# Kernel tuning notes

Hardware: AMD Instinct MI355X
Metric: run time of the kernel (lower is better)

The kernel has to match this reference:

```python
import math
import jax, jax.numpy as jnp
import numpy as np

B, N, D, H = 4, 2048, 512, 8
HD = D // H


def setup_inputs() -> dict:
    key = jax.random.key(0)
    ks = jax.random.split(key, 7)
    w_scale = 1.0 / math.sqrt(D)  # keep logits in a sane range (like default init)
    return {
        "q": jax.random.normal(ks[0], (B, N, D), dtype=jnp.float32),
        "mask": jax.random.randint(ks[1], (B, N), 0, 2) == 1,  # True = masked key
        "attn_bias": jax.random.normal(ks[2], (B, N, N), dtype=jnp.float32),
        "Wq": jax.random.normal(ks[3], (D, D), dtype=jnp.float32) * w_scale,
        "Wk": jax.random.normal(ks[4], (D, D), dtype=jnp.float32) * w_scale,
        "Wv": jax.random.normal(ks[5], (D, D), dtype=jnp.float32) * w_scale,
        "Wo": jax.random.normal(ks[6], (D, D), dtype=jnp.float32) * w_scale,
    }


def _heads(v):
    # [B, N, D] -> [H, B, N, HD]  (mirrors reshape + movedim(-2, 0))
    b, n, d = v.shape
    return v.reshape(b, n, H, HD).transpose(2, 0, 1, 3)


def reference(q, mask, attn_bias, Wq, Wk, Wv, Wo):
    # Linear projections (torch Linear: x @ W.T)
    qh = _heads(q @ Wq.T)
    kh = _heads(q @ Wk.T)   # self-attention: h defaults to q
    vh = _heads(q @ Wv.T)
    # scores: [H, B, Nq, Nk]
    scores = jnp.einsum("hbqd,hbkd->hbqk", qh, kh) / math.sqrt(HD)
    scores = scores + attn_bias[None]                     # broadcast over heads
    scores = jnp.where(mask[None, :, None, :], -jnp.inf, scores)
    attn = jax.nn.softmax(scores, axis=-1)
    out = jnp.einsum("hbqk,hbkd->hbqd", attn, vh)         # [H, B, Nq, HD]
    out = out.transpose(1, 2, 0, 3).reshape(q.shape[0], q.shape[1], D)
    return out @ Wo.T
```

## Files before the change

### kernel.cpp

```cpp
#include <hip/hip_runtime.h>
#include <stdint.h>


typedef __attribute__((ext_vector_type(8))) short short8;
typedef __attribute__((ext_vector_type(4))) short short4v;
typedef __attribute__((ext_vector_type(4))) float f32x4;

#define DEV static __device__ __forceinline__

constexpr int Bc = 4, Nc = 2048, Dc = 512, Hc = 8, HDc = 64;
constexpr int Mc = Bc * Nc;
constexpr int QKVNc = 3 * Dc;
constexpr float L2E = 1.44269504f;

DEV short bf16cast(float f) {
  return (short)__builtin_bit_cast(unsigned short, (__bf16)f);
}
DEV unsigned cvt_pk_bf16(float a, float b) {
  unsigned short lb = __builtin_bit_cast(unsigned short, (__bf16)a);
  unsigned short hb = __builtin_bit_cast(unsigned short, (__bf16)b);
  return (unsigned)lb | ((unsigned)hb << 16);
}
DEV unsigned pack_shorts(short a, short b) {
  return (unsigned)(unsigned short)a | ((unsigned)(unsigned short)b << 16);
}
DEV short8 cvt8(float4 a, float4 b) {
  union { short8 s; uint4 u; } r;
  r.u.x = cvt_pk_bf16(a.x, a.y); r.u.y = cvt_pk_bf16(a.z, a.w);
  r.u.z = cvt_pk_bf16(b.x, b.y); r.u.w = cvt_pk_bf16(b.z, b.w);
  return r.s;
}
DEV float fast_exp2(float x) {
#if __has_builtin(__builtin_amdgcn_exp2f)
  return __builtin_amdgcn_exp2f(x);
#else
  return exp2f(x);
#endif
}
DEV void permswap32(unsigned& a, unsigned& b) {
  asm volatile("v_permlane32_swap_b32 %0, %1" : "+v"(a), "+v"(b));
}

__global__ void cvtw_kernel(const float* __restrict__ Wq, const float* __restrict__ Wk,
                            const float* __restrict__ Wv, const float* __restrict__ Wo,
                            short* __restrict__ Wqkv, short* __restrict__ Wob) {
  int which = blockIdx.x >> 8;
  int j = (blockIdx.x & 255) * 256 + threadIdx.x;
  const float* src = which == 0 ? Wq : which == 1 ? Wk : which == 2 ? Wv : Wo;
  short* dst = (which == 3) ? Wob : Wqkv + which * (Dc * Dc);
  float4 v = ((const float4*)src)[j];
  short4v o = { bf16cast(v.x), bf16cast(v.y), bf16cast(v.z), bf16cast(v.w) };
  ((short4v*)dst)[j] = o;
}

__global__ void maskprep_kernel(const void* __restrict__ mask, float* __restrict__ mf) {
  __shared__ int flag;
  if (threadIdx.x == 0) flag = 0;
  __syncthreads();
  const uchar4* m4 = (const uchar4*)mask;
  int acc = 0;
  for (int i = threadIdx.x; i < 2048; i += 1024) {
    uchar4 v = m4[i];
    acc |= (int)v.y | (int)v.z | (int)v.w;
  }
  if (acc) atomicOr(&flag, 1);
  __syncthreads();
  int isbyte = flag;
  for (int i = threadIdx.x; i < Bc * Nc; i += 1024) {
    int v = isbyte ? (int)((const unsigned char*)mask)[i] : ((const int*)mask)[i];
    mf[i] = v ? -1e30f : 0.0f;
  }
}

template<bool A_F32, bool OUT_F32>
__global__ __launch_bounds__(256, 2) void gemm_bt(const void* __restrict__ Av,
                                                  const short* __restrict__ Bm,
                                                  void* __restrict__ Cv,
                                                  int M, int N, int K,
                                                  int qcols, float cscale) {
  __shared__ __align__(16) short At[128 * 72];
  __shared__ __align__(16) short Bt[128 * 72];
  const int tid = threadIdx.x, lane = tid & 63, wv = tid >> 6;
  const int quad = lane >> 4, l16 = lane & 15;
  const int mbase = blockIdx.y * 128, nbase = blockIdx.x * 128;
  const int wr = (wv >> 1) * 64, wc = (wv & 1) * 64;
  const float scale = (nbase < qcols) ? cscale : 1.0f;
  f32x4 acc[4][4] = {};
  float4 apf[4][2]; short8 aph[4], bpre[4];
#pragma unroll
  for (int i = 0; i < 4; i++) {
    int flat = i * 256 + tid, row = flat >> 3, ch8 = (flat & 7) * 8;
    if (A_F32) {
      const float* Af = (const float*)Av;
      apf[i][0] = *(const float4*)&Af[(size_t)(mbase + row) * K + ch8];
      apf[i][1] = *(const float4*)&Af[(size_t)(mbase + row) * K + ch8 + 4];
    } else {
      aph[i] = *(const short8*)&((const short*)Av)[(size_t)(mbase + row) * K + ch8];
    }
    bpre[i] = *(const short8*)&Bm[(size_t)(nbase + row) * K + ch8];
  }
  for (int k0 = 0; k0 < K; k0 += 64) {
    __syncthreads();
#pragma unroll
    for (int i = 0; i < 4; i++) {
      int flat = i * 256 + tid, row = flat >> 3, ch8 = (flat & 7) * 8;
      *(short8*)&At[row * 72 + ch8] = A_F32 ? cvt8(apf[i][0], apf[i][1]) : aph[i];
      *(short8*)&Bt[row * 72 + ch8] = bpre[i];
    }
    if (k0 + 64 < K) {
#pragma unroll
      for (int i = 0; i < 4; i++) {
        int flat = i * 256 + tid, row = flat >> 3, ch8 = (flat & 7) * 8;
        if (A_F32) {
          const float* Af = (const float*)Av;
          apf[i][0] = *(const float4*)&Af[(size_t)(mbase + row) * K + k0 + 64 + ch8];
          apf[i][1] = *(const float4*)&Af[(size_t)(mbase + row) * K + k0 + 64 + ch8 + 4];
        } else {
          aph[i] = *(const short8*)&((const short*)Av)[(size_t)(mbase + row) * K + k0 + 64 + ch8];
        }
        bpre[i] = *(const short8*)&Bm[(size_t)(nbase + row) * K + k0 + 64 + ch8];
      }
    }
    __syncthreads();
#pragma unroll
    for (int s = 0; s < 2; s++) {
      short8 af[4], bf[4];
#pragma unroll
      for (int t = 0; t < 4; t++) {
        af[t] = *(short8*)&At[(wr + t * 16 + l16) * 72 + quad * 8 + s * 32];
        bf[t] = *(short8*)&Bt[(wc + t * 16 + l16) * 72 + quad * 8 + s * 32];
      }
#pragma unroll
      for (int mt = 0; mt < 4; mt++)
#pragma unroll
        for (int nt = 0; nt < 4; nt++)
          acc[mt][nt] = __builtin_amdgcn_mfma_f32_16x16x32_bf16(af[mt], bf[nt], acc[mt][nt], 0, 0, 0);
    }
  }
#pragma unroll
  for (int mt = 0; mt < 4; mt++)
#pragma unroll
    for (int nt = 0; nt < 4; nt++)
#pragma unroll
      for (int r = 0; r < 4; r++) {
        int row = mbase + wr + mt * 16 + quad * 4 + r;
        int col = nbase + wc + nt * 16 + l16;
        float v = acc[mt][nt][r] * scale;
        if (OUT_F32) ((float*)Cv)[(size_t)row * N + col] = v;
        else         ((short*)Cv)[(size_t)row * N + col] = bf16cast(v);
      }
}

__global__ __launch_bounds__(256, 2) void attn_kernel(const short* __restrict__ QKV,
                                                      const float* __restrict__ bias,
                                                      const float* __restrict__ maskf,
                                                      short* __restrict__ Aout) {
  __shared__ __align__(16) short Kt[2][64 * 64];
  __shared__ __align__(16) short Vt[2][64 * 64];
  __shared__ __align__(16) float mlds[Nc];
  const int tid = threadIdx.x, lane = tid & 63, wv = tid >> 6;
  const int quad = lane >> 4, l16 = lane & 15;
  const int qt = blockIdx.x & 15, h = (blockIdx.x >> 4) & 7, b = (int)(blockIdx.x >> 7);
  const int qrow0 = qt * 128;
  const int q0 = qrow0 + wv * 32 + l16;
  const float* biasq0 = bias + ((size_t)b * Nc + q0) * Nc;
  const float* biasq1 = biasq0 + (size_t)16 * Nc;

  ((float4*)mlds)[tid]       = ((const float4*)(maskf + b * Nc))[tid];
  ((float4*)mlds)[tid + 256] = ((const float4*)(maskf + b * Nc))[tid + 256];

  short8 qf[2][2];
  {
    const short* qp0 = QKV + (size_t)(b * Nc + q0) * QKVNc + h * HDc + quad * 8;
    qf[0][0] = *(const short8*)qp0;
    qf[0][1] = *(const short8*)(qp0 + 32);
    const short* qp1 = qp0 + (size_t)16 * QKVNc;
    qf[1][0] = *(const short8*)qp1;
    qf[1][1] = *(const short8*)(qp1 + 32);
  }

  const int krow = tid >> 2, kch0 = (tid & 3) * 2;
  const int kw0 = krow * 64 + ((kch0 ^ (krow & 7)) << 3);
  const int kw1 = krow * 64 + (((kch0 + 1) ^ (krow & 7)) << 3);
  const int vp = tid & 31, vq = tid >> 5;
  const int vperm = (vp & 25) | ((vp & 4) >> 1) | ((vp & 2) << 1);
  const int vwbase = (((vperm >> 2)) << 3) + 2 * (vperm & 3);
  const short* Kbase = QKV + Dc + h * HDc;
  const short* Vbase = QKV + 2 * Dc + h * HDc;

  short8 kpre0, kpre1, v0pre, v1pre;
  {
    const short* kp = &Kbase[(size_t)(b * Nc + krow) * QKVNc + kch0 * 8];
    kpre0 = *(const short8*)kp;
    kpre1 = *(const short8*)(kp + 8);
    v0pre = *(const short8*)&Vbase[(size_t)(b * Nc + 2 * vp) * QKVNc + vq * 8];
    v1pre = *(const short8*)&Vbase[(size_t)(b * Nc + 2 * vp + 1) * QKVNc + vq * 8];
  }

  const short ONEB = (short)0x3F80;
  const short8 ones = { ONEB, ONEB, ONEB, ONEB, ONEB, ONEB, ONEB, ONEB };

  f32x4 oacc[2][4] = {};
  f32x4 sumacc[2] = {};

  for (int kt = 0; kt < 32; kt++) {
    const int cur = kt & 1;
    const int kb = kt * 64;
    const int kbn = ((kt + 1) & 31) * 64;

    *(short8*)&Kt[cur][kw0] = kpre0;
    *(short8*)&Kt[cur][kw1] = kpre1;
#pragma unroll
    for (int j = 0; j < 8; j++) {
      int hd = vq * 8 + j;
      *(unsigned*)&Vt[cur][hd * 64 + (vwbase ^ ((hd & 7) << 3))] =
          pack_shorts(v0pre[j], v1pre[j]);
    }
    __syncthreads();

    {
      const short* kp = &Kbase[(size_t)(b * Nc + kbn + krow) * QKVNc + kch0 * 8];
      kpre0 = *(const short8*)kp;
      kpre1 = *(const short8*)(kp + 8);
      v0pre = *(const short8*)&Vbase[(size_t)(b * Nc + kbn + 2 * vp) * QKVNc + vq * 8];
      v1pre = *(const short8*)&Vbase[(size_t)(b * Nc + kbn + 2 * vp + 1) * QKVNc + vq * 8];
    }
    float4 bb[2][4];
#pragma unroll
    for (int t = 0; t < 4; t++) {
      bb[0][t] = *(const float4*)&biasq0[kb + t * 16 + quad * 4];
      bb[1][t] = *(const float4*)&biasq1[kb + t * 16 + quad * 4];
    }

    f32x4 sacc[2][4];
#pragma unroll
    for (int t = 0; t < 4; t++) {
      float4 mv = *(const float4*)&mlds[kb + t * 16 + quad * 4];
      sacc[0][t][0] = mv.x; sacc[0][t][1] = mv.y; sacc[0][t][2] = mv.z; sacc[0][t][3] = mv.w;
      sacc[1][t] = sacc[0][t];
    }

#pragma unroll
    for (int s = 0; s < 2; s++)
#pragma unroll
      for (int t = 0; t < 4; t++) {
        short8 kf = *(short8*)&Kt[cur][(t * 16 + l16) * 64 + (((quad + 4 * s) ^ (l16 & 7)) << 3)];
        sacc[0][t] = __builtin_amdgcn_mfma_f32_16x16x32_bf16(kf, qf[0][s], sacc[0][t], 0, 0, 0);
        sacc[1][t] = __builtin_amdgcn_mfma_f32_16x16x32_bf16(kf, qf[1][s], sacc[1][t], 0, 0, 0);
      }

    short8 pf[2][2];
#pragma unroll
    for (int n = 0; n < 2; n++) {
      unsigned pw[4][2];
#pragma unroll
      for (int t = 0; t < 4; t++) {
        float p0 = fast_exp2(__builtin_fmaf(bb[n][t].x, L2E, sacc[n][t][0]));
        float p1 = fast_exp2(__builtin_fmaf(bb[n][t].y, L2E, sacc[n][t][1]));
        float p2 = fast_exp2(__builtin_fmaf(bb[n][t].z, L2E, sacc[n][t][2]));
        float p3 = fast_exp2(__builtin_fmaf(bb[n][t].w, L2E, sacc[n][t][3]));
        pw[t][0] = cvt_pk_bf16(p0, p1);
        pw[t][1] = cvt_pk_bf16(p2, p3);
      }
      permswap32(pw[0][0], pw[1][0]); permswap32(pw[0][1], pw[1][1]);
      permswap32(pw[2][0], pw[3][0]); permswap32(pw[2][1], pw[3][1]);
      union { unsigned u[4]; short8 s; }
          a0{{pw[0][0], pw[0][1], pw[1][0], pw[1][1]}},
          a1{{pw[2][0], pw[2][1], pw[3][0], pw[3][1]}};
      pf[n][0] = a0.s; pf[n][1] = a1.s;
    }

#pragma unroll
    for (int s = 0; s < 2; s++) {
      sumacc[0] = __builtin_amdgcn_mfma_f32_16x16x32_bf16(pf[0][s], ones, sumacc[0], 0, 0, 0);
      sumacc[1] = __builtin_amdgcn_mfma_f32_16x16x32_bf16(pf[1][s], ones, sumacc[1], 0, 0, 0);
#pragma unroll
      for (int t = 0; t < 4; t++) {
        short8 vf = *(short8*)&Vt[cur][(t * 16 + l16) * 64 + (((quad + 4 * s) ^ (l16 & 7)) << 3)];
        oacc[0][t] = __builtin_amdgcn_mfma_f32_16x16x32_bf16(pf[0][s], vf, oacc[0][t], 0, 0, 0);
        oacc[1][t] = __builtin_amdgcn_mfma_f32_16x16x32_bf16(pf[1][s], vf, oacc[1][t], 0, 0, 0);
      }
    }
  }

#pragma unroll
  for (int m = 0; m < 2; m++)
#pragma unroll
    for (int r = 0; r < 4; r++) {
      float inv = 1.0f / sumacc[m][r];
      int row = b * Nc + qrow0 + wv * 32 + m * 16 + quad * 4 + r;
#pragma unroll
      for (int t = 0; t < 4; t++)
        Aout[(size_t)row * Dc + h * HDc + t * 16 + l16] = bf16cast(oacc[m][t][r] * inv);
    }
}

extern "C" void kernel_launch(void* const* d_in, const int* in_sizes, int n_in,
                              void* d_out, int out_size, void* d_ws, size_t ws_size,
                              hipStream_t stream) {
  const float* q    = (const float*)d_in[0];
  const void*  mask = d_in[1];
  const float* bias = (const float*)d_in[2];
  const float* Wq   = (const float*)d_in[3];
  const float* Wk   = (const float*)d_in[4];
  const float* Wv   = (const float*)d_in[5];
  const float* Wo   = (const float*)d_in[6];
  float* out = (float*)d_out;

  char* ws = (char*)d_ws;
  short* Wqkv = (short*)ws;  ws += (size_t)QKVNc * Dc * 2;
  short* Wob  = (short*)ws;  ws += (size_t)Dc * Dc * 2;
  float* mf   = (float*)ws;  ws += (size_t)Bc * Nc * 4;
  short* QKV  = (short*)ws;  ws += (size_t)Mc * QKVNc * 2;
  short* aout = (short*)ws;  ws += (size_t)Mc * Dc * 2;

  cvtw_kernel<<<dim3(1024), dim3(256), 0, stream>>>(Wq, Wk, Wv, Wo, Wqkv, Wob);
  maskprep_kernel<<<dim3(1), dim3(1024), 0, stream>>>(mask, mf);

  gemm_bt<true, false><<<dim3(QKVNc / 128, Mc / 128), dim3(256), 0, stream>>>(
      (const void*)q, Wqkv, (void*)QKV, Mc, QKVNc, Dc, Dc, 0.125f * L2E);
  attn_kernel<<<dim3(Bc * Hc * 16), dim3(256), 0, stream>>>(QKV, bias, mf, aout);
  gemm_bt<false, true><<<dim3(Dc / 128, Mc / 128), dim3(256), 0, stream>>>(
      (const void*)aout, Wob, (void*)out, Mc, Dc, Dc, 0, 1.0f);
}
```

Measured before the change: 273.0 us.

## Fuse weight/mask prep into GEMM and attention, async K loads, bias prefetch

Removes the separate weight-conversion and mask-prep kernels: the GEMMs now read fp32 weights directly and convert them in-register, and each attention block builds its mask row in LDS itself. The attention kernel loads K tiles straight into LDS with global_load_lds double buffering, prefetches the next tile's bias one iteration ahead, and raises wave priority around the MFMA sections. The output GEMM switches to a 64-wide N tile to launch more blocks. The trade-off is redundant weight conversion and mask scanning per block, plus higher register pressure from the bias prefetch.

```diff
diff --git a/kernel.cpp b/kernel.cpp
--- a/kernel.cpp
+++ b/kernel.cpp
@@ -40,53 +40,37 @@
 DEV void permswap32(unsigned& a, unsigned& b) {
   asm volatile("v_permlane32_swap_b32 %0, %1" : "+v"(a), "+v"(b));
 }
-
-__global__ void cvtw_kernel(const float* __restrict__ Wq, const float* __restrict__ Wk,
-                            const float* __restrict__ Wv, const float* __restrict__ Wo,
-                            short* __restrict__ Wqkv, short* __restrict__ Wob) {
-  int which = blockIdx.x >> 8;
-  int j = (blockIdx.x & 255) * 256 + threadIdx.x;
-  const float* src = which == 0 ? Wq : which == 1 ? Wk : which == 2 ? Wv : Wo;
-  short* dst = (which == 3) ? Wob : Wqkv + which * (Dc * Dc);
-  float4 v = ((const float4*)src)[j];
-  short4v o = { bf16cast(v.x), bf16cast(v.y), bf16cast(v.z), bf16cast(v.w) };
-  ((short4v*)dst)[j] = o;
-}
-
-__global__ void maskprep_kernel(const void* __restrict__ mask, float* __restrict__ mf) {
-  __shared__ int flag;
-  if (threadIdx.x == 0) flag = 0;
-  __syncthreads();
-  const uchar4* m4 = (const uchar4*)mask;
-  int acc = 0;
-  for (int i = threadIdx.x; i < 2048; i += 1024) {
-    uchar4 v = m4[i];
-    acc |= (int)v.y | (int)v.z | (int)v.w;
-  }
-  if (acc) atomicOr(&flag, 1);
-  __syncthreads();
-  int isbyte = flag;
-  for (int i = threadIdx.x; i < Bc * Nc; i += 1024) {
-    int v = isbyte ? (int)((const unsigned char*)mask)[i] : ((const int*)mask)[i];
-    mf[i] = v ? -1e30f : 0.0f;
-  }
-}
-
-template<bool A_F32, bool OUT_F32>
+DEV void gl_lds16(const short* g, short* l) {
+  __builtin_amdgcn_global_load_lds(
+      (const __attribute__((address_space(1))) void*)g,
+      (__attribute__((address_space(3))) void*)l, 16, 0, 0);
+}
+
+template<bool A_F32, int BN, bool OUT_F32>
 __global__ __launch_bounds__(256, 2) void gemm_bt(const void* __restrict__ Av,
-                                                  const short* __restrict__ Bm,
+                                                  const float* __restrict__ B0,
+                                                  const float* __restrict__ B1,
+                                                  const float* __restrict__ B2,
                                                   void* __restrict__ Cv,
-                                                  int M, int N, int K,
+                                                  int M, int N,
                                                   int qcols, float cscale) {
+  constexpr int K = 512;
+  constexpr int BG = BN / 32;
+  constexpr int MT = (BN == 128) ? 4 : 2;
+  constexpr int NT = 4;
   __shared__ __align__(16) short At[128 * 72];
-  __shared__ __align__(16) short Bt[128 * 72];
+  __shared__ __align__(16) short Bt[BN * 72];
   const int tid = threadIdx.x, lane = tid & 63, wv = tid >> 6;
   const int quad = lane >> 4, l16 = lane & 15;
-  const int mbase = blockIdx.y * 128, nbase = blockIdx.x * 128;
-  const int wr = (wv >> 1) * 64, wc = (wv & 1) * 64;
+  const int mbase = blockIdx.y * 128, nbase = blockIdx.x * BN;
+  const int wr = (BN == 128) ? (wv >> 1) * 64 : wv * 32;
+  const int wc = (BN == 128) ? (wv & 1) * 64 : 0;
+  const float* Bsel = nbase < 512 ? B0 : (nbase < 1024 ? B1 : B2);
+  const int col0 = nbase & 511;
   const float scale = (nbase < qcols) ? cscale : 1.0f;
-  f32x4 acc[4][4] = {};
-  float4 apf[4][2]; short8 aph[4], bpre[4];
+  f32x4 acc[MT][NT] = {};
+  float4 apf[4][2]; short8 aph[4];
+  float4 bpf[BG][2];
 #pragma unroll
   for (int i = 0; i < 4; i++) {
     int flat = i * 256 + tid, row = flat >> 3, ch8 = (flat & 7) * 8;
@@ -97,7 +81,12 @@
     } else {
       aph[i] = *(const short8*)&((const short*)Av)[(size_t)(mbase + row) * K + ch8];
     }
-    bpre[i] = *(const short8*)&Bm[(size_t)(nbase + row) * K + ch8];
+  }
+#pragma unroll
+  for (int i = 0; i < BG; i++) {
+    int flat = i * 256 + tid, row = flat >> 3, ch8 = (flat & 7) * 8;
+    bpf[i][0] = *(const float4*)&Bsel[(size_t)(col0 + row) * K + ch8];
+    bpf[i][1] = *(const float4*)&Bsel[(size_t)(col0 + row) * K + ch8 + 4];
   }
   for (int k0 = 0; k0 < K; k0 += 64) {
     __syncthreads();
@@ -105,7 +94,11 @@
     for (int i = 0; i < 4; i++) {
       int flat = i * 256 + tid, row = flat >> 3, ch8 = (flat & 7) * 8;
       *(short8*)&At[row * 72 + ch8] = A_F32 ? cvt8(apf[i][0], apf[i][1]) : aph[i];
-      *(short8*)&Bt[row * 72 + ch8] = bpre[i];
+    }
+#pragma unroll
+    for (int i = 0; i < BG; i++) {
+      int flat = i * 256 + tid, row = flat >> 3, ch8 = (flat & 7) * 8;
+      *(short8*)&Bt[row * 72 + ch8] = cvt8(bpf[i][0], bpf[i][1]);
     }
     if (k0 + 64 < K) {
 #pragma unroll
@@ -118,29 +111,35 @@
         } else {
           aph[i] = *(const short8*)&((const short*)Av)[(size_t)(mbase + row) * K + k0 + 64 + ch8];
         }
-        bpre[i] = *(const short8*)&Bm[(size_t)(nbase + row) * K + k0 + 64 + ch8];
+      }
+#pragma unroll
+      for (int i = 0; i < BG; i++) {
+        int flat = i * 256 + tid, row = flat >> 3, ch8 = (flat & 7) * 8;
+        bpf[i][0] = *(const float4*)&Bsel[(size_t)(col0 + row) * K + k0 + 64 + ch8];
+        bpf[i][1] = *(const float4*)&Bsel[(size_t)(col0 + row) * K + k0 + 64 + ch8 + 4];
       }
     }
     __syncthreads();
 #pragma unroll
     for (int s = 0; s < 2; s++) {
-      short8 af[4], bf[4];
-#pragma unroll
-      for (int t = 0; t < 4; t++) {
+      short8 af[MT], bf[NT];
+#pragma unroll
+      for (int t = 0; t < MT; t++)
         af[t] = *(short8*)&At[(wr + t * 16 + l16) * 72 + quad * 8 + s * 32];
+#pragma unroll
+      for (int t = 0; t < NT; t++)
         bf[t] = *(short8*)&Bt[(wc + t * 16 + l16) * 72 + quad * 8 + s * 32];
-      }
-#pragma unroll
-      for (int mt = 0; mt < 4; mt++)
-#pragma unroll
-        for (int nt = 0; nt < 4; nt++)
+#pragma unroll
+      for (int mt = 0; mt < MT; mt++)
+#pragma unroll
+        for (int nt = 0; nt < NT; nt++)
           acc[mt][nt] = __builtin_amdgcn_mfma_f32_16x16x32_bf16(af[mt], bf[nt], acc[mt][nt], 0, 0, 0);
     }
   }
 #pragma unroll
-  for (int mt = 0; mt < 4; mt++)
-#pragma unroll
-    for (int nt = 0; nt < 4; nt++)
+  for (int mt = 0; mt < MT; mt++)
+#pragma unroll
+    for (int nt = 0; nt < NT; nt++)
 #pragma unroll
       for (int r = 0; r < 4; r++) {
         int row = mbase + wr + mt * 16 + quad * 4 + r;
@@ -153,11 +152,12 @@
 
 __global__ __launch_bounds__(256, 2) void attn_kernel(const short* __restrict__ QKV,
                                                       const float* __restrict__ bias,
-                                                      const float* __restrict__ maskf,
+                                                      const void* __restrict__ mask,
                                                       short* __restrict__ Aout) {
   __shared__ __align__(16) short Kt[2][64 * 64];
   __shared__ __align__(16) short Vt[2][64 * 64];
   __shared__ __align__(16) float mlds[Nc];
+  __shared__ int mflag;
   const int tid = threadIdx.x, lane = tid & 63, wv = tid >> 6;
   const int quad = lane >> 4, l16 = lane & 15;
   const int qt = blockIdx.x & 15, h = (blockIdx.x >> 4) & 7, b = (int)(blockIdx.x >> 7);
@@ -165,9 +165,16 @@
   const int q0 = qrow0 + wv * 32 + l16;
   const float* biasq0 = bias + ((size_t)b * Nc + q0) * Nc;
   const float* biasq1 = biasq0 + (size_t)16 * Nc;
-
-  ((float4*)mlds)[tid]       = ((const float4*)(maskf + b * Nc))[tid];
-  ((float4*)mlds)[tid + 256] = ((const float4*)(maskf + b * Nc))[tid + 256];
+  const short* Kbase = QKV + Dc + h * HDc;
+  const short* Vbase = QKV + 2 * Dc + h * HDc;
+
+#pragma unroll
+  for (int j = 0; j < 2; j++) {
+    int seg = wv * 2 + j, c = seg * 64 + lane;
+    int row = c >> 3, ch = c & 7;
+    gl_lds16(&Kbase[(size_t)(b * Nc + row) * QKVNc + ((ch ^ (row & 7)) << 3)],
+             &Kt[0][seg * 512]);
+  }
 
   short8 qf[2][2];
   {
@@ -179,22 +186,41 @@
     qf[1][1] = *(const short8*)(qp1 + 32);
   }
 
-  const int krow = tid >> 2, kch0 = (tid & 3) * 2;
-  const int kw0 = krow * 64 + ((kch0 ^ (krow & 7)) << 3);
-  const int kw1 = krow * 64 + (((kch0 + 1) ^ (krow & 7)) << 3);
   const int vp = tid & 31, vq = tid >> 5;
   const int vperm = (vp & 25) | ((vp & 4) >> 1) | ((vp & 2) << 1);
   const int vwbase = (((vperm >> 2)) << 3) + 2 * (vperm & 3);
-  const short* Kbase = QKV + Dc + h * HDc;
-  const short* Vbase = QKV + 2 * Dc + h * HDc;
-
-  short8 kpre0, kpre1, v0pre, v1pre;
+
+  short8 v0pre, v1pre;
+  v0pre = *(const short8*)&Vbase[(size_t)(b * Nc + 2 * vp) * QKVNc + vq * 8];
+  v1pre = *(const short8*)&Vbase[(size_t)(b * Nc + 2 * vp + 1) * QKVNc + vq * 8];
+  float4 bpre[2][4];
+#pragma unroll
+  for (int t = 0; t < 4; t++) {
+    bpre[0][t] = *(const float4*)&biasq0[t * 16 + quad * 4];
+    bpre[1][t] = *(const float4*)&biasq1[t * 16 + quad * 4];
+  }
+
+  if (tid == 0) mflag = 0;
+  __syncthreads();
   {
-    const short* kp = &Kbase[(size_t)(b * Nc + krow) * QKVNc + kch0 * 8];
-    kpre0 = *(const short8*)kp;
-    kpre1 = *(const short8*)(kp + 8);
-    v0pre = *(const short8*)&Vbase[(size_t)(b * Nc + 2 * vp) * QKVNc + vq * 8];
-    v1pre = *(const short8*)&Vbase[(size_t)(b * Nc + 2 * vp + 1) * QKVNc + vq * 8];
+    const uchar4* mw = (const uchar4*)((const char*)mask + (size_t)b * 2048);
+    int acc = 0;
+#pragma unroll
+    for (int i = tid; i < 512; i += 256) {
+      uchar4 v = mw[i];
+      acc |= (int)v.y | (int)v.z | (int)v.w;
+    }
+    if (acc) atomicOr(&mflag, 1);
+  }
+  __syncthreads();
+  {
+    int isbyte = mflag;
+    const unsigned char* mb = (const unsigned char*)mask + (size_t)b * 2048;
+    const int* mi = (const int*)mask + (size_t)b * 2048;
+    for (int i = tid; i < Nc; i += 256) {
+      int v = isbyte ? (int)mb[i] : mi[i];
+      mlds[i] = v ? -1e30f : 0.0f;
+    }
   }
 
   const short ONEB = (short)0x3F80;
@@ -204,12 +230,10 @@
   f32x4 sumacc[2] = {};
 
   for (int kt = 0; kt < 32; kt++) {
-    const int cur = kt & 1;
+    const int cur = kt & 1, nxt = cur ^ 1;
     const int kb = kt * 64;
     const int kbn = ((kt + 1) & 31) * 64;
 
-    *(short8*)&Kt[cur][kw0] = kpre0;
-    *(short8*)&Kt[cur][kw1] = kpre1;
 #pragma unroll
     for (int j = 0; j < 8; j++) {
       int hd = vq * 8 + j;
@@ -218,19 +242,15 @@
     }
     __syncthreads();
 
-    {
-      const short* kp = &Kbase[(size_t)(b * Nc + kbn + krow) * QKVNc + kch0 * 8];
-      kpre0 = *(const short8*)kp;
-      kpre1 = *(const short8*)(kp + 8);
-      v0pre = *(const short8*)&Vbase[(size_t)(b * Nc + kbn + 2 * vp) * QKVNc + vq * 8];
-      v1pre = *(const short8*)&Vbase[(size_t)(b * Nc + kbn + 2 * vp + 1) * QKVNc + vq * 8];
-    }
-    float4 bb[2][4];
-#pragma unroll
-    for (int t = 0; t < 4; t++) {
-      bb[0][t] = *(const float4*)&biasq0[kb + t * 16 + quad * 4];
-      bb[1][t] = *(const float4*)&biasq1[kb + t * 16 + quad * 4];
-    }
+#pragma unroll
+    for (int j = 0; j < 2; j++) {
+      int seg = wv * 2 + j, c = seg * 64 + lane;
+      int row = c >> 3, ch = c & 7;
+      gl_lds16(&Kbase[(size_t)(b * Nc + kbn + row) * QKVNc + ((ch ^ (row & 7)) << 3)],
+               &Kt[nxt][seg * 512]);
+    }
+    v0pre = *(const short8*)&Vbase[(size_t)(b * Nc + kbn + 2 * vp) * QKVNc + vq * 8];
+    v1pre = *(const short8*)&Vbase[(size_t)(b * Nc + kbn + 2 * vp + 1) * QKVNc + vq * 8];
 
     f32x4 sacc[2][4];
 #pragma unroll
@@ -240,6 +260,7 @@
       sacc[1][t] = sacc[0][t];
     }
 
+    __builtin_amdgcn_s_setprio(1);
 #pragma unroll
     for (int s = 0; s < 2; s++)
 #pragma unroll
@@ -248,6 +269,7 @@
         sacc[0][t] = __builtin_amdgcn_mfma_f32_16x16x32_bf16(kf, qf[0][s], sacc[0][t], 0, 0, 0);
         sacc[1][t] = __builtin_amdgcn_mfma_f32_16x16x32_bf16(kf, qf[1][s], sacc[1][t], 0, 0, 0);
       }
+    __builtin_amdgcn_s_setprio(0);
 
     short8 pf[2][2];
 #pragma unroll
@@ -255,10 +277,10 @@
       unsigned pw[4][2];
 #pragma unroll
       for (int t = 0; t < 4; t++) {
-        float p0 = fast_exp2(__builtin_fmaf(bb[n][t].x, L2E, sacc[n][t][0]));
-        float p1 = fast_exp2(__builtin_fmaf(bb[n][t].y, L2E, sacc[n][t][1]));
-        float p2 = fast_exp2(__builtin_fmaf(bb[n][t].z, L2E, sacc[n][t][2]));
-        float p3 = fast_exp2(__builtin_fmaf(bb[n][t].w, L2E, sacc[n][t][3]));
+        float p0 = fast_exp2(__builtin_fmaf(bpre[n][t].x, L2E, sacc[n][t][0]));
+        float p1 = fast_exp2(__builtin_fmaf(bpre[n][t].y, L2E, sacc[n][t][1]));
+        float p2 = fast_exp2(__builtin_fmaf(bpre[n][t].z, L2E, sacc[n][t][2]));
+        float p3 = fast_exp2(__builtin_fmaf(bpre[n][t].w, L2E, sacc[n][t][3]));
         pw[t][0] = cvt_pk_bf16(p0, p1);
         pw[t][1] = cvt_pk_bf16(p2, p3);
       }
@@ -271,6 +293,13 @@
     }
 
 #pragma unroll
+    for (int t = 0; t < 4; t++) {
+      bpre[0][t] = *(const float4*)&biasq0[kbn + t * 16 + quad * 4];
+      bpre[1][t] = *(const float4*)&biasq1[kbn + t * 16 + quad * 4];
+    }
+
+    __builtin_amdgcn_s_setprio(1);
+#pragma unroll
     for (int s = 0; s < 2; s++) {
       sumacc[0] = __builtin_amdgcn_mfma_f32_16x16x32_bf16(pf[0][s], ones, sumacc[0], 0, 0, 0);
       sumacc[1] = __builtin_amdgcn_mfma_f32_16x16x32_bf16(pf[1][s], ones, sumacc[1], 0, 0, 0);
@@ -281,6 +310,7 @@
         oacc[1][t] = __builtin_amdgcn_mfma_f32_16x16x32_bf16(pf[1][s], vf, oacc[1][t], 0, 0, 0);
       }
     }
+    __builtin_amdgcn_s_setprio(0);
   }
 
 #pragma unroll
@@ -308,18 +338,12 @@
   float* out = (float*)d_out;
 
   char* ws = (char*)d_ws;
-  short* Wqkv = (short*)ws;  ws += (size_t)QKVNc * Dc * 2;
-  short* Wob  = (short*)ws;  ws += (size_t)Dc * Dc * 2;
-  float* mf   = (float*)ws;  ws += (size_t)Bc * Nc * 4;
   short* QKV  = (short*)ws;  ws += (size_t)Mc * QKVNc * 2;
   short* aout = (short*)ws;  ws += (size_t)Mc * Dc * 2;
 
-  cvtw_kernel<<<dim3(1024), dim3(256), 0, stream>>>(Wq, Wk, Wv, Wo, Wqkv, Wob);
-  maskprep_kernel<<<dim3(1), dim3(1024), 0, stream>>>(mask, mf);
-
-  gemm_bt<true, false><<<dim3(QKVNc / 128, Mc / 128), dim3(256), 0, stream>>>(
-      (const void*)q, Wqkv, (void*)QKV, Mc, QKVNc, Dc, Dc, 0.125f * L2E);
-  attn_kernel<<<dim3(Bc * Hc * 16), dim3(256), 0, stream>>>(QKV, bias, mf, aout);
-  gemm_bt<false, true><<<dim3(Dc / 128, Mc / 128), dim3(256), 0, stream>>>(
-      (const void*)aout, Wob, (void*)out, Mc, Dc, Dc, 0, 1.0f);
-}
+  gemm_bt<true, 128, false><<<dim3(QKVNc / 128, Mc / 128), dim3(256), 0, stream>>>(
+      (const void*)q, Wq, Wk, Wv, (void*)QKV, Mc, QKVNc, Dc, 0.125f * L2E);
+  attn_kernel<<<dim3(Bc * Hc * 16), dim3(256), 0, stream>>>(QKV, bias, mask, aout);
+  gemm_bt<false, 64, true><<<dim3(Dc / 64, Mc / 128), dim3(256), 0, stream>>>(
+      (const void*)aout, Wo, Wo, Wo, (void*)out, Mc, Dc, 0, 1.0f);
+}
```

After: 256.4 us. 6.1% less time.
